# Performance work log

Measured on AMD Instinct MI355X. Metric: run time of the kernel, lower is better.

The kernel has to match this reference:

```python
import jax, jax.numpy as jnp
import numpy as np

N_NODES = 50000


def _sage_conv(x, src, dst, Wl, Wr, b):
    """SAGEConv with mean aggregation: lin_l(mean_j x_j) + lin_r(x_i) + b."""
    msgs = x[src]                                                # [E, Din] gather
    agg = jax.ops.segment_sum(msgs, dst, num_segments=N_NODES)  # [N, Din] scatter-add
    cnt = jax.ops.segment_sum(jnp.ones((src.shape[0], 1), x.dtype), dst,
                              num_segments=N_NODES)             # [N, 1]
    agg = agg / jnp.maximum(cnt, 1.0)                           # mean
    return agg @ Wl.T + x @ Wr.T + b                            # [N, Dout]


def setup_inputs() -> dict:
    key = jax.random.key(0)
    ks = jax.random.split(key, 8)
    d_in, d_h = 64, 128
    x = jax.random.normal(ks[0], (N_NODES, d_in), dtype=jnp.float32)
    edge_index = jax.random.randint(ks[1], (2, 800000), 0, N_NODES, dtype=jnp.int32)
    s1 = 1.0 / np.sqrt(d_in)
    s2 = 1.0 / np.sqrt(d_h)
    return {
        "x": x,
        "edge_index": edge_index,
        "Wl1": jax.random.normal(ks[2], (d_h, d_in), dtype=jnp.float32) * s1,
        "Wr1": jax.random.normal(ks[3], (d_h, d_in), dtype=jnp.float32) * s1,
        "b1": jnp.zeros((d_h,), dtype=jnp.float32),
        "Wl2": jax.random.normal(ks[4], (d_h, d_h), dtype=jnp.float32) * s2,
        "Wr2": jax.random.normal(ks[5], (d_h, d_h), dtype=jnp.float32) * s2,
        "b2": jnp.zeros((d_h,), dtype=jnp.float32),
    }


def reference(x, edge_index, Wl1, Wr1, b1, Wl2, Wr2, b2):
    src, dst = edge_index[0], edge_index[1]
    # layer 1: conv -> dropout(eval: identity) -> ReLU
    h = jax.nn.relu(_sage_conv(x, src, dst, Wl1, Wr1, b1))
    # layer 2
    h = jax.nn.relu(_sage_conv(h, src, dst, Wl2, Wr2, b2))
    return h
```

## Files before the change

### kernel.cpp

```cpp
#include <hip/hip_runtime.h>

#define N_NODES 50000
#define NBUCK 782
#define BCAP 2048
#define BSHIFT 11

typedef __attribute__((ext_vector_type(8))) short short8;
typedef __attribute__((ext_vector_type(4))) float floatx4;
typedef __attribute__((ext_vector_type(2))) float floatx2;
typedef __attribute__((ext_vector_type(2))) int intx2;

static __device__ __forceinline__ unsigned short f2bf(float f) {
  unsigned int u = __builtin_bit_cast(unsigned int, f);
  u += 0x7fff + ((u >> 16) & 1);
  return (unsigned short)(u >> 16);
}
static __device__ __forceinline__ void fp8x8_acc(intx2 v, floatx2* ac) {
  ac[0] += __builtin_amdgcn_cvt_pk_f32_fp8(v[0], false);
  ac[1] += __builtin_amdgcn_cvt_pk_f32_fp8(v[0], true);
  ac[2] += __builtin_amdgcn_cvt_pk_f32_fp8(v[1], false);
  ac[3] += __builtin_amdgcn_cvt_pk_f32_fp8(v[1], true);
}


__global__ void __launch_bounds__(512) prep_scatter(
    const float* __restrict__ x,
    const float* __restrict__ Wl1, const float* __restrict__ Wr1,
    const float* __restrict__ Wl2, const float* __restrict__ Wr2,
    unsigned short* __restrict__ xb, unsigned char* __restrict__ xq,
    unsigned short* __restrict__ W1, unsigned short* __restrict__ W2,
    const int* __restrict__ src, const int* __restrict__ dst,
    int* __restrict__ bucket_cur, int* __restrict__ buf, int E, int n) {
  const int t = threadIdx.x;
  const int gid = blockIdx.x * 512 + t;
  const int gsz = gridDim.x * 512;
  for (int i = gid; i < n * 16; i += gsz) {
    float4 v = ((const float4*)x)[i];
    unsigned int lo = (unsigned int)f2bf(v.x) | ((unsigned int)f2bf(v.y) << 16);
    unsigned int hi = (unsigned int)f2bf(v.z) | ((unsigned int)f2bf(v.w) << 16);
    ((uint2*)xb)[i] = make_uint2(lo, hi);
    int q = __builtin_amdgcn_cvt_pk_fp8_f32(v.x, v.y, 0, false);
    q = __builtin_amdgcn_cvt_pk_fp8_f32(v.z, v.w, q, true);
    ((int*)xq)[i] = q;
  }
  {
    unsigned char* h1q = xq + ((size_t)n + 1) * 64;
    if (gid < 16) ((int*)(xq + (size_t)n * 64))[gid] = 0;
    if (gid >= 16 && gid < 48) ((int*)(h1q + (size_t)n * 128))[gid - 16] = 0;
  }
  for (int i = gid; i < 128 * 128; i += gsz) {
    int c = i >> 7, k = i & 127;
    W1[i] = f2bf(k < 64 ? Wl1[c * 64 + k] : Wr1[c * 64 + k - 64]);
  }
  for (int i = gid; i < 128 * 256; i += gsz) {
    int c = i >> 8, k = i & 255;
    W2[i] = f2bf(k < 128 ? Wl2[c * 128 + k] : Wr2[c * 128 + k - 128]);
  }

  __shared__ int hist[NBUCK];
  __shared__ int base_s[NBUCK];
  for (int i = t; i < NBUCK; i += 512) hist[i] = 0;
  __syncthreads();
  int e0 = blockIdx.x * 4096;
  int sv[8], dv[8], bv[8];
#pragma unroll
  for (int p = 0; p < 8; ++p) {
    int e = e0 + p * 512 + t;
    if (e < E) {
      sv[p] = src[e];
      dv[p] = dst[e];
      bv[p] = dv[p] >> 6;
      atomicAdd(&hist[bv[p]], 1);
    } else bv[p] = -1;
  }
  __syncthreads();
  for (int i = t; i < NBUCK; i += 512) {
    int c = hist[i];
    base_s[i] = c > 0 ? atomicAdd(&bucket_cur[i], c) : 0;
  }
  __syncthreads();
  for (int i = t; i < NBUCK; i += 512) hist[i] = 0;
  __syncthreads();
#pragma unroll
  for (int p = 0; p < 8; ++p) {
    if (bv[p] >= 0) {
      int sub = base_s[bv[p]] + atomicAdd(&hist[bv[p]], 1);
      if (sub < BCAP) buf[(bv[p] << BSHIFT) + sub] = (sv[p] << 6) | (dv[p] & 63);
    }
  }
}


__global__ void __launch_bounds__(512, 6) csr_agg_gemm1(
    int* __restrict__ buf, const int* __restrict__ bucket_cur,
    int* __restrict__ row_start, int* __restrict__ row_cnt,
    const unsigned short* __restrict__ xb, const unsigned char* __restrict__ xq,
    const unsigned short* __restrict__ W1, const float* __restrict__ b1,
    unsigned short* __restrict__ h1, unsigned char* __restrict__ h1q, int n) {
  __shared__ int eb[BCAP];
  __shared__ int gsrc[BCAP];
  __shared__ __align__(16) unsigned short aggS[64 * 72];
  __shared__ int cnt[64];
  __shared__ int tmp[64];
  __shared__ int cur[64];
  const int t = threadIdx.x;
  const int b = blockIdx.x;
  const int node0 = b << 6;
  const int len = min(bucket_cur[b], BCAP);
  int* reg = buf + (b << BSHIFT);

  if (t < 64) cnt[t] = 0;
  __syncthreads();
  for (int i = t; i < len; i += 512) {
    int p = reg[i];
    eb[i] = p;
    atomicAdd(&cnt[p & 63], 1);
  }
  __syncthreads();
  if (t < 64) tmp[t] = (cnt[t] + 7) & ~7;
  __syncthreads();
#pragma unroll
  for (int off = 1; off < 64; off <<= 1) {
    int u = (t >= off && t < 64) ? tmp[t - off] : 0;
    __syncthreads();
    if (t < 64) tmp[t] += u;
    __syncthreads();
  }
  if (t < 64) {
    int c8 = (cnt[t] + 7) & ~7;
    int ex = tmp[t] - c8;
    cur[t] = ex;
    int nd = node0 + t;
    if (nd < n) {
      row_start[nd] = (b << BSHIFT) + ex;
      row_cnt[nd] = cnt[t];
    }
  }
  __syncthreads();
  for (int i = t; i < len; i += 512) {
    int p = eb[i];
    int sub = atomicAdd(&cur[p & 63], 1);
    int s = p >> 6;
    if (sub < BCAP) { gsrc[sub] = s; reg[sub] = s; }
  }
  __syncthreads();
  if (t < 64) {
    int c8 = (cnt[t] + 7) & ~7;
    int e1 = tmp[t];
    for (int j = e1 - c8 + cnt[t]; j < e1; ++j)
      if (j < BCAP) { gsrc[j] = n; reg[j] = n; }
  }
  __syncthreads();

  const int lane = t & 63;
  const int wv = t >> 6;
  const int eq = lane >> 3;
  const int cl = lane & 7;
#pragma unroll 1
  for (int p = 0; p < 4; ++p) {
    int locA = wv + p * 16;
    int locB = locA + 8;
    int cnA = cnt[locA], cnB = cnt[locB];
    int cpA = (cnA + 7) & ~7, cpB = (cnB + 7) & ~7;
    int baseA = tmp[locA] - cpA;
    int baseB = tmp[locB] - cpB;
    floatx2 aA[4], aB[4];
#pragma unroll
    for (int j = 0; j < 4; ++j) { aA[j] = (floatx2){0.f, 0.f}; aB[j] = (floatx2){0.f, 0.f}; }
    int mx = max(cpA, cpB);
    int sA = (0 < cpA) ? gsrc[baseA + eq] : n;
    int sB = (0 < cpB) ? gsrc[baseB + eq] : n;
    intx2 vA = *(const intx2*)(xq + (size_t)sA * 64 + cl * 8);
    intx2 vB = *(const intx2*)(xq + (size_t)sB * 64 + cl * 8);
    for (int e = 8; e < mx; e += 8) {
      int sA1 = (e < cpA) ? gsrc[baseA + e + eq] : n;
      int sB1 = (e < cpB) ? gsrc[baseB + e + eq] : n;
      intx2 vA1 = *(const intx2*)(xq + (size_t)sA1 * 64 + cl * 8);
      intx2 vB1 = *(const intx2*)(xq + (size_t)sB1 * 64 + cl * 8);
      fp8x8_acc(vA, aA);
      fp8x8_acc(vB, aB);
      vA = vA1; vB = vB1;
    }
    fp8x8_acc(vA, aA);
    fp8x8_acc(vB, aB);
    float rA[8], rB[8];
#pragma unroll
    for (int j = 0; j < 4; ++j) {
      rA[2 * j] = aA[j][0]; rA[2 * j + 1] = aA[j][1];
      rB[2 * j] = aB[j][0]; rB[2 * j + 1] = aB[j][1];
    }
#pragma unroll
    for (int j = 0; j < 8; ++j) {
      rA[j] += __shfl_xor(rA[j], 8, 64);
      rA[j] += __shfl_xor(rA[j], 16, 64);
      rA[j] += __shfl_xor(rA[j], 32, 64);
      rB[j] += __shfl_xor(rB[j], 8, 64);
      rB[j] += __shfl_xor(rB[j], 16, 64);
      rB[j] += __shfl_xor(rB[j], 32, 64);
    }
    if (eq == 0) {
      float invA = 1.0f / (float)max(cnA, 1);
      float invB = 1.0f / (float)max(cnB, 1);
      short8 oA, oB;
#pragma unroll
      for (int j = 0; j < 8; ++j) { oA[j] = (short)f2bf(rA[j] * invA); oB[j] = (short)f2bf(rB[j] * invB); }
      *(short8*)(aggS + locA * 72 + cl * 8) = oA;
      *(short8*)(aggS + locB * 72 + cl * 8) = oB;
    }
  }
  __syncthreads();

  const int m = lane & 15;
  const int q = lane >> 4;
  const int rw = (wv & 1) * 32;
  const int cw = (wv >> 1) * 32;
  floatx4 acc[2][2];
#pragma unroll
  for (int rt = 0; rt < 2; ++rt)
#pragma unroll
    for (int ct = 0; ct < 2; ++ct) acc[rt][ct] = (floatx4){0.f, 0.f, 0.f, 0.f};

  int ra = node0 + rw + m;      if (ra > n - 1) ra = n - 1;
  int rb = node0 + rw + 16 + m; if (rb > n - 1) rb = n - 1;
  const unsigned short* selfA0 = xb + (size_t)ra * 64 + q * 8;
  const unsigned short* selfA1 = xb + (size_t)rb * 64 + q * 8;
  const unsigned short* aggL0 = aggS + (rw + m) * 72 + q * 8;
  const unsigned short* aggL1 = aggS + (rw + 16 + m) * 72 + q * 8;
  const unsigned short* Wc0 = W1 + (size_t)(cw + m) * 128 + q * 8;
  const unsigned short* Wc1 = W1 + (size_t)(cw + 16 + m) * 128 + q * 8;

#pragma unroll
  for (int kc = 0; kc < 2; ++kc) {
    short8 a0 = *(const short8*)(aggL0 + kc * 32);
    short8 a1 = *(const short8*)(aggL1 + kc * 32);
    short8 w0 = *(const short8*)(Wc0 + kc * 32);
    short8 w1 = *(const short8*)(Wc1 + kc * 32);
    acc[0][0] = __builtin_amdgcn_mfma_f32_16x16x32_bf16(a0, w0, acc[0][0], 0, 0, 0);
    acc[0][1] = __builtin_amdgcn_mfma_f32_16x16x32_bf16(a0, w1, acc[0][1], 0, 0, 0);
    acc[1][0] = __builtin_amdgcn_mfma_f32_16x16x32_bf16(a1, w0, acc[1][0], 0, 0, 0);
    acc[1][1] = __builtin_amdgcn_mfma_f32_16x16x32_bf16(a1, w1, acc[1][1], 0, 0, 0);
  }
#pragma unroll
  for (int kc = 0; kc < 2; ++kc) {
    short8 a0 = *(const short8*)(selfA0 + kc * 32);
    short8 a1 = *(const short8*)(selfA1 + kc * 32);
    short8 w0 = *(const short8*)(Wc0 + 64 + kc * 32);
    short8 w1 = *(const short8*)(Wc1 + 64 + kc * 32);
    acc[0][0] = __builtin_amdgcn_mfma_f32_16x16x32_bf16(a0, w0, acc[0][0], 0, 0, 0);
    acc[0][1] = __builtin_amdgcn_mfma_f32_16x16x32_bf16(a0, w1, acc[0][1], 0, 0, 0);
    acc[1][0] = __builtin_amdgcn_mfma_f32_16x16x32_bf16(a1, w0, acc[1][0], 0, 0, 0);
    acc[1][1] = __builtin_amdgcn_mfma_f32_16x16x32_bf16(a1, w1, acc[1][1], 0, 0, 0);
  }

  float bv0 = b1[cw + m], bv1 = b1[cw + 16 + m];
#pragma unroll
  for (int rt = 0; rt < 2; ++rt) {
#pragma unroll
    for (int j = 0; j < 4; ++j) {
      int row = node0 + rw + rt * 16 + q * 4 + j;
      if (row < n) {
        float v0 = acc[rt][0][j] + bv0; v0 = v0 > 0.f ? v0 : 0.f;
        float v1 = acc[rt][1][j] + bv1; v1 = v1 > 0.f ? v1 : 0.f;
        h1[(size_t)row * 128 + cw + m] = f2bf(v0);
        h1[(size_t)row * 128 + cw + 16 + m] = f2bf(v1);
        h1q[(size_t)row * 128 + cw + m] =
            (unsigned char)__builtin_amdgcn_cvt_pk_fp8_f32(v0, v0, 0, false);
        h1q[(size_t)row * 128 + cw + 16 + m] =
            (unsigned char)__builtin_amdgcn_cvt_pk_fp8_f32(v1, v1, 0, false);
      }
    }
  }
}


__global__ void __launch_bounds__(512, 6) agg_gemm2(
    const unsigned short* __restrict__ h1, const unsigned char* __restrict__ h1q,
    const int* __restrict__ row_start, const int* __restrict__ row_cnt,
    const int* __restrict__ buf, const unsigned short* __restrict__ W2,
    const float* __restrict__ b2, float* __restrict__ out, int n) {
  __shared__ int gsrcS[BCAP];
  __shared__ __align__(16) unsigned short aggS[64 * 136];
  const int t = threadIdx.x;
  const int lane = t & 63;
  const int wv = t >> 6;
  const int node0 = blockIdx.x << 6;

  {
    const int4* b4 = (const int4*)(buf + ((size_t)blockIdx.x << BSHIFT));
    ((int4*)gsrcS)[t] = b4[t];
  }
  __syncthreads();

  const int eq = lane >> 4;
  const int cl = lane & 15;
#pragma unroll 1
  for (int lp = 0; lp < 4; ++lp) {
    int locA = wv + lp * 16;
    int locB = locA + 8;
    int ndA = node0 + locA, ndB = node0 + locB;
    int cnA = 0, stA = 0, cnB = 0, stB = 0;
    if (ndA < n) { cnA = row_cnt[ndA]; stA = row_start[ndA] - (blockIdx.x << BSHIFT); }
    if (ndB < n) { cnB = row_cnt[ndB]; stB = row_start[ndB] - (blockIdx.x << BSHIFT); }
    int cpA = (cnA + 7) & ~7, cpB = (cnB + 7) & ~7;
    int mx = max(cpA, cpB);
    floatx2 aA[4], aB[4];
#pragma unroll
    for (int j = 0; j < 4; ++j) { aA[j] = (floatx2){0.f, 0.f}; aB[j] = (floatx2){0.f, 0.f}; }
    int sA0 = (0 < cpA) ? gsrcS[stA + eq] : n;
    int sA1 = (0 < cpA) ? gsrcS[stA + 4 + eq] : n;
    int sB0 = (0 < cpB) ? gsrcS[stB + eq] : n;
    int sB1 = (0 < cpB) ? gsrcS[stB + 4 + eq] : n;
    intx2 vA0 = *(const intx2*)(h1q + (size_t)sA0 * 128 + cl * 8);
    intx2 vA1 = *(const intx2*)(h1q + (size_t)sA1 * 128 + cl * 8);
    intx2 vB0 = *(const intx2*)(h1q + (size_t)sB0 * 128 + cl * 8);
    intx2 vB1 = *(const intx2*)(h1q + (size_t)sB1 * 128 + cl * 8);
    for (int e = 8; e < mx; e += 8) {
      int tA0 = (e < cpA) ? gsrcS[stA + e + eq] : n;
      int tA1 = (e < cpA) ? gsrcS[stA + e + 4 + eq] : n;
      int tB0 = (e < cpB) ? gsrcS[stB + e + eq] : n;
      int tB1 = (e < cpB) ? gsrcS[stB + e + 4 + eq] : n;
      intx2 wA0 = *(const intx2*)(h1q + (size_t)tA0 * 128 + cl * 8);
      intx2 wA1 = *(const intx2*)(h1q + (size_t)tA1 * 128 + cl * 8);
      intx2 wB0 = *(const intx2*)(h1q + (size_t)tB0 * 128 + cl * 8);
      intx2 wB1 = *(const intx2*)(h1q + (size_t)tB1 * 128 + cl * 8);
      fp8x8_acc(vA0, aA); fp8x8_acc(vA1, aA);
      fp8x8_acc(vB0, aB); fp8x8_acc(vB1, aB);
      vA0 = wA0; vA1 = wA1; vB0 = wB0; vB1 = wB1;
    }
    fp8x8_acc(vA0, aA); fp8x8_acc(vA1, aA);
    fp8x8_acc(vB0, aB); fp8x8_acc(vB1, aB);

    float rA[8], rB[8];
#pragma unroll
    for (int j = 0; j < 4; ++j) {
      rA[2 * j] = aA[j][0]; rA[2 * j + 1] = aA[j][1];
      rB[2 * j] = aB[j][0]; rB[2 * j + 1] = aB[j][1];
    }
#pragma unroll
    for (int j = 0; j < 8; ++j) {
      rA[j] += __shfl_xor(rA[j], 16, 64);
      rA[j] += __shfl_xor(rA[j], 32, 64);
      rB[j] += __shfl_xor(rB[j], 16, 64);
      rB[j] += __shfl_xor(rB[j], 32, 64);
    }
    if (eq == 0) {
      float invA = 1.0f / (float)max(cnA, 1);
      float invB = 1.0f / (float)max(cnB, 1);
      short8 oA, oB;
#pragma unroll
      for (int j = 0; j < 8; ++j) { oA[j] = (short)f2bf(rA[j] * invA); oB[j] = (short)f2bf(rB[j] * invB); }
      *(short8*)(aggS + locA * 136 + cl * 8) = oA;
      *(short8*)(aggS + locB * 136 + cl * 8) = oB;
    }
  }
  __syncthreads();

  const int m = lane & 15;
  const int q = lane >> 4;
  const int rw = (wv & 1) * 32;
  const int cw = (wv >> 1) * 32;
  floatx4 acc[2][2];
#pragma unroll
  for (int rt = 0; rt < 2; ++rt)
#pragma unroll
    for (int ct = 0; ct < 2; ++ct) acc[rt][ct] = (floatx4){0.f, 0.f, 0.f, 0.f};

  int ra = node0 + rw + m;      if (ra > n - 1) ra = n - 1;
  int rb = node0 + rw + 16 + m; if (rb > n - 1) rb = n - 1;
  const unsigned short* selfA0 = h1 + (size_t)ra * 128 + q * 8;
  const unsigned short* selfA1 = h1 + (size_t)rb * 128 + q * 8;
  const unsigned short* aggL0 = aggS + (rw + m) * 136 + q * 8;
  const unsigned short* aggL1 = aggS + (rw + 16 + m) * 136 + q * 8;
  const unsigned short* Wc0 = W2 + (size_t)(cw + m) * 256 + q * 8;
  const unsigned short* Wc1 = W2 + (size_t)(cw + 16 + m) * 256 + q * 8;

#pragma unroll
  for (int kc = 0; kc < 4; ++kc) {
    short8 a0 = *(const short8*)(aggL0 + kc * 32);
    short8 a1 = *(const short8*)(aggL1 + kc * 32);
    short8 w0 = *(const short8*)(Wc0 + kc * 32);
    short8 w1 = *(const short8*)(Wc1 + kc * 32);
    acc[0][0] = __builtin_amdgcn_mfma_f32_16x16x32_bf16(a0, w0, acc[0][0], 0, 0, 0);
    acc[0][1] = __builtin_amdgcn_mfma_f32_16x16x32_bf16(a0, w1, acc[0][1], 0, 0, 0);
    acc[1][0] = __builtin_amdgcn_mfma_f32_16x16x32_bf16(a1, w0, acc[1][0], 0, 0, 0);
    acc[1][1] = __builtin_amdgcn_mfma_f32_16x16x32_bf16(a1, w1, acc[1][1], 0, 0, 0);
  }
#pragma unroll
  for (int kc = 0; kc < 4; ++kc) {
    short8 a0 = *(const short8*)(selfA0 + kc * 32);
    short8 a1 = *(const short8*)(selfA1 + kc * 32);
    short8 w0 = *(const short8*)(Wc0 + 128 + kc * 32);
    short8 w1 = *(const short8*)(Wc1 + 128 + kc * 32);
    acc[0][0] = __builtin_amdgcn_mfma_f32_16x16x32_bf16(a0, w0, acc[0][0], 0, 0, 0);
    acc[0][1] = __builtin_amdgcn_mfma_f32_16x16x32_bf16(a0, w1, acc[0][1], 0, 0, 0);
    acc[1][0] = __builtin_amdgcn_mfma_f32_16x16x32_bf16(a1, w0, acc[1][0], 0, 0, 0);
    acc[1][1] = __builtin_amdgcn_mfma_f32_16x16x32_bf16(a1, w1, acc[1][1], 0, 0, 0);
  }

  float bv0 = b2[cw + m], bv1 = b2[cw + 16 + m];
#pragma unroll
  for (int rt = 0; rt < 2; ++rt) {
#pragma unroll
    for (int j = 0; j < 4; ++j) {
      int row = node0 + rw + rt * 16 + q * 4 + j;
      if (row < n) {
        float v0 = acc[rt][0][j] + bv0; v0 = v0 > 0.f ? v0 : 0.f;
        float v1 = acc[rt][1][j] + bv1; v1 = v1 > 0.f ? v1 : 0.f;
        out[(size_t)row * 128 + cw + m] = v0;
        out[(size_t)row * 128 + cw + 16 + m] = v1;
      }
    }
  }
}


extern "C" void kernel_launch(void* const* d_in, const int* in_sizes, int n_in,
                              void* d_out, int out_size, void* d_ws, size_t ws_size,
                              hipStream_t stream) {
  const int N = N_NODES;
  const int E = in_sizes[1] / 2;
  const float* x   = (const float*)d_in[0];
  const int*   src = (const int*)d_in[1];
  const int*   dst = src + E;
  const float* Wl1 = (const float*)d_in[2];
  const float* Wr1 = (const float*)d_in[3];
  const float* b1  = (const float*)d_in[4];
  const float* Wl2 = (const float*)d_in[5];
  const float* Wr2 = (const float*)d_in[6];
  const float* b2  = (const float*)d_in[7];
  float* out = (float*)d_out;

  unsigned short* xb = (unsigned short*)d_ws;
  unsigned short* h1 = xb + (size_t)N * 64;
  unsigned short* W1 = h1 + (size_t)N * 128;
  unsigned short* W2 = W1 + 128 * 128;
  int* row_start  = (int*)(W2 + 128 * 256);
  int* row_cnt    = row_start + N;
  int* bucket_cur = row_cnt + N;
  int* buf        = bucket_cur + 784;
  unsigned char* xq  = (unsigned char*)(buf + (size_t)NBUCK * BCAP);
  unsigned char* h1q = xq + ((size_t)N + 1) * 64;

  (void)hipMemsetAsync(bucket_cur, 0, NBUCK * sizeof(int), stream);
  int sb = (E + 4095) / 4096;
  prep_scatter<<<sb, 512, 0, stream>>>(x, Wl1, Wr1, Wl2, Wr2, xb, xq, W1, W2,
                                       src, dst, bucket_cur, buf, E, N);
  csr_agg_gemm1<<<NBUCK, 512, 0, stream>>>(buf, bucket_cur, row_start, row_cnt,
                                           xb, xq, W1, b1, h1, h1q, N);
  agg_gemm2<<<NBUCK, 512, 0, stream>>>(h1, h1q, row_start, row_cnt, buf, W2, b2, out, N);
}
```

Baseline: 185.1 us.

## Halve node buckets to 32 nodes with 256-thread blocks and 4-way gather ILP

Buckets now cover 32 destination nodes instead of 64, which doubles the block count to 1563 and halves the threads per block to 256 for both aggregation+GEMM kernels. Each wave now aggregates four nodes at once instead of two, giving more independent gather loads in flight. The GEMM tiling is remapped so each wave covers all 32 rows for a 32-column slice. Bucket capacity drops to 1024 edges, which leaves less headroom before edges overflow and get dropped for heavily connected buckets.

```diff
diff --git a/kernel.cpp b/kernel.cpp
--- a/kernel.cpp
+++ b/kernel.cpp
@@ -1,9 +1,9 @@
 #include <hip/hip_runtime.h>
 
 #define N_NODES 50000
-#define NBUCK 782
-#define BCAP 2048
-#define BSHIFT 11
+#define NBUCK 1563
+#define BCAP 1024
+#define BSHIFT 10
 
 typedef __attribute__((ext_vector_type(8))) short short8;
 typedef __attribute__((ext_vector_type(4))) float floatx4;
@@ -69,7 +69,7 @@
     if (e < E) {
       sv[p] = src[e];
       dv[p] = dst[e];
-      bv[p] = dv[p] >> 6;
+      bv[p] = dv[p] >> 5;
       atomicAdd(&hist[bv[p]], 1);
     } else bv[p] = -1;
   }
@@ -85,13 +85,13 @@
   for (int p = 0; p < 8; ++p) {
     if (bv[p] >= 0) {
       int sub = base_s[bv[p]] + atomicAdd(&hist[bv[p]], 1);
-      if (sub < BCAP) buf[(bv[p] << BSHIFT) + sub] = (sv[p] << 6) | (dv[p] & 63);
-    }
-  }
-}
-
-
-__global__ void __launch_bounds__(512, 6) csr_agg_gemm1(
+      if (sub < BCAP) buf[(bv[p] << BSHIFT) + sub] = (sv[p] << 5) | (dv[p] & 31);
+    }
+  }
+}
+
+
+__global__ void __launch_bounds__(256) csr_agg_gemm1(
     int* __restrict__ buf, const int* __restrict__ bucket_cur,
     int* __restrict__ row_start, int* __restrict__ row_cnt,
     const unsigned short* __restrict__ xb, const unsigned char* __restrict__ xq,
@@ -99,34 +99,34 @@
     unsigned short* __restrict__ h1, unsigned char* __restrict__ h1q, int n) {
   __shared__ int eb[BCAP];
   __shared__ int gsrc[BCAP];
-  __shared__ __align__(16) unsigned short aggS[64 * 72];
-  __shared__ int cnt[64];
-  __shared__ int tmp[64];
-  __shared__ int cur[64];
+  __shared__ __align__(16) unsigned short aggS[32 * 72];
+  __shared__ int cnt[32];
+  __shared__ int tmp[32];
+  __shared__ int cur[32];
   const int t = threadIdx.x;
   const int b = blockIdx.x;
-  const int node0 = b << 6;
+  const int node0 = b << 5;
   const int len = min(bucket_cur[b], BCAP);
   int* reg = buf + (b << BSHIFT);
 
-  if (t < 64) cnt[t] = 0;
-  __syncthreads();
-  for (int i = t; i < len; i += 512) {
+  if (t < 32) cnt[t] = 0;
+  __syncthreads();
+  for (int i = t; i < len; i += 256) {
     int p = reg[i];
     eb[i] = p;
-    atomicAdd(&cnt[p & 63], 1);
-  }
-  __syncthreads();
-  if (t < 64) tmp[t] = (cnt[t] + 7) & ~7;
-  __syncthreads();
-#pragma unroll
-  for (int off = 1; off < 64; off <<= 1) {
-    int u = (t >= off && t < 64) ? tmp[t - off] : 0;
+    atomicAdd(&cnt[p & 31], 1);
+  }
+  __syncthreads();
+  if (t < 32) tmp[t] = (cnt[t] + 7) & ~7;
+  __syncthreads();
+#pragma unroll
+  for (int off = 1; off < 32; off <<= 1) {
+    int u = (t >= off && t < 32) ? tmp[t - off] : 0;
     __syncthreads();
-    if (t < 64) tmp[t] += u;
+    if (t < 32) tmp[t] += u;
     __syncthreads();
   }
-  if (t < 64) {
+  if (t < 32) {
     int c8 = (cnt[t] + 7) & ~7;
     int ex = tmp[t] - c8;
     cur[t] = ex;
@@ -137,14 +137,14 @@
     }
   }
   __syncthreads();
-  for (int i = t; i < len; i += 512) {
+  for (int i = t; i < len; i += 256) {
     int p = eb[i];
-    int sub = atomicAdd(&cur[p & 63], 1);
-    int s = p >> 6;
+    int sub = atomicAdd(&cur[p & 31], 1);
+    int s = p >> 5;
     if (sub < BCAP) { gsrc[sub] = s; reg[sub] = s; }
   }
   __syncthreads();
-  if (t < 64) {
+  if (t < 32) {
     int c8 = (cnt[t] + 7) & ~7;
     int e1 = tmp[t];
     for (int j = e1 - c8 + cnt[t]; j < e1; ++j)
@@ -157,75 +157,79 @@
   const int eq = lane >> 3;
   const int cl = lane & 7;
 #pragma unroll 1
-  for (int p = 0; p < 4; ++p) {
-    int locA = wv + p * 16;
-    int locB = locA + 8;
-    int cnA = cnt[locA], cnB = cnt[locB];
-    int cpA = (cnA + 7) & ~7, cpB = (cnB + 7) & ~7;
-    int baseA = tmp[locA] - cpA;
-    int baseB = tmp[locB] - cpB;
-    floatx2 aA[4], aB[4];
-#pragma unroll
-    for (int j = 0; j < 4; ++j) { aA[j] = (floatx2){0.f, 0.f}; aB[j] = (floatx2){0.f, 0.f}; }
-    int mx = max(cpA, cpB);
-    int sA = (0 < cpA) ? gsrc[baseA + eq] : n;
-    int sB = (0 < cpB) ? gsrc[baseB + eq] : n;
-    intx2 vA = *(const intx2*)(xq + (size_t)sA * 64 + cl * 8);
-    intx2 vB = *(const intx2*)(xq + (size_t)sB * 64 + cl * 8);
+  for (int g = 0; g < 2; ++g) {
+    int loc0 = wv * 8 + g * 4;
+    int cn0 = cnt[loc0], cn1 = cnt[loc0 + 1], cn2 = cnt[loc0 + 2], cn3 = cnt[loc0 + 3];
+    int cp0 = (cn0 + 7) & ~7, cp1 = (cn1 + 7) & ~7, cp2 = (cn2 + 7) & ~7, cp3 = (cn3 + 7) & ~7;
+    int ba0 = tmp[loc0] - cp0, ba1 = tmp[loc0 + 1] - cp1,
+        ba2 = tmp[loc0 + 2] - cp2, ba3 = tmp[loc0 + 3] - cp3;
+    floatx2 a0[4], a1[4], a2[4], a3[4];
+#pragma unroll
+    for (int j = 0; j < 4; ++j) {
+      a0[j] = (floatx2){0.f, 0.f}; a1[j] = (floatx2){0.f, 0.f};
+      a2[j] = (floatx2){0.f, 0.f}; a3[j] = (floatx2){0.f, 0.f};
+    }
+    int mx = max(max(cp0, cp1), max(cp2, cp3));
+    int s0 = (0 < cp0) ? gsrc[ba0 + eq] : n;
+    int s1 = (0 < cp1) ? gsrc[ba1 + eq] : n;
+    int s2 = (0 < cp2) ? gsrc[ba2 + eq] : n;
+    int s3 = (0 < cp3) ? gsrc[ba3 + eq] : n;
+    intx2 v0 = *(const intx2*)(xq + (size_t)s0 * 64 + cl * 8);
+    intx2 v1 = *(const intx2*)(xq + (size_t)s1 * 64 + cl * 8);
+    intx2 v2 = *(const intx2*)(xq + (size_t)s2 * 64 + cl * 8);
+    intx2 v3 = *(const intx2*)(xq + (size_t)s3 * 64 + cl * 8);
     for (int e = 8; e < mx; e += 8) {
-      int sA1 = (e < cpA) ? gsrc[baseA + e + eq] : n;
-      int sB1 = (e < cpB) ? gsrc[baseB + e + eq] : n;
-      intx2 vA1 = *(const intx2*)(xq + (size_t)sA1 * 64 + cl * 8);
-      intx2 vB1 = *(const intx2*)(xq + (size_t)sB1 * 64 + cl * 8);
-      fp8x8_acc(vA, aA);
-      fp8x8_acc(vB, aB);
-      vA = vA1; vB = vB1;
-    }
-    fp8x8_acc(vA, aA);
-    fp8x8_acc(vB, aB);
-    float rA[8], rB[8];
-#pragma unroll
-    for (int j = 0; j < 4; ++j) {
-      rA[2 * j] = aA[j][0]; rA[2 * j + 1] = aA[j][1];
-      rB[2 * j] = aB[j][0]; rB[2 * j + 1] = aB[j][1];
-    }
-#pragma unroll
-    for (int j = 0; j < 8; ++j) {
-      rA[j] += __shfl_xor(rA[j], 8, 64);
-      rA[j] += __shfl_xor(rA[j], 16, 64);
-      rA[j] += __shfl_xor(rA[j], 32, 64);
-      rB[j] += __shfl_xor(rB[j], 8, 64);
-      rB[j] += __shfl_xor(rB[j], 16, 64);
-      rB[j] += __shfl_xor(rB[j], 32, 64);
-    }
-    if (eq == 0) {
-      float invA = 1.0f / (float)max(cnA, 1);
-      float invB = 1.0f / (float)max(cnB, 1);
-      short8 oA, oB;
-#pragma unroll
-      for (int j = 0; j < 8; ++j) { oA[j] = (short)f2bf(rA[j] * invA); oB[j] = (short)f2bf(rB[j] * invB); }
-      *(short8*)(aggS + locA * 72 + cl * 8) = oA;
-      *(short8*)(aggS + locB * 72 + cl * 8) = oB;
+      int u0 = (e < cp0) ? gsrc[ba0 + e + eq] : n;
+      int u1 = (e < cp1) ? gsrc[ba1 + e + eq] : n;
+      int u2 = (e < cp2) ? gsrc[ba2 + e + eq] : n;
+      int u3 = (e < cp3) ? gsrc[ba3 + e + eq] : n;
+      intx2 w0 = *(const intx2*)(xq + (size_t)u0 * 64 + cl * 8);
+      intx2 w1 = *(const intx2*)(xq + (size_t)u1 * 64 + cl * 8);
+      intx2 w2 = *(const intx2*)(xq + (size_t)u2 * 64 + cl * 8);
+      intx2 w3 = *(const intx2*)(xq + (size_t)u3 * 64 + cl * 8);
+      fp8x8_acc(v0, a0); fp8x8_acc(v1, a1); fp8x8_acc(v2, a2); fp8x8_acc(v3, a3);
+      v0 = w0; v1 = w1; v2 = w2; v3 = w3;
+    }
+    fp8x8_acc(v0, a0); fp8x8_acc(v1, a1); fp8x8_acc(v2, a2); fp8x8_acc(v3, a3);
+#pragma unroll
+    for (int i = 0; i < 4; ++i) {
+      floatx2* ai = (i == 0) ? a0 : (i == 1) ? a1 : (i == 2) ? a2 : a3;
+      int cni = (i == 0) ? cn0 : (i == 1) ? cn1 : (i == 2) ? cn2 : cn3;
+      float r[8];
+#pragma unroll
+      for (int j = 0; j < 4; ++j) { r[2 * j] = ai[j][0]; r[2 * j + 1] = ai[j][1]; }
+#pragma unroll
+      for (int j = 0; j < 8; ++j) {
+        r[j] += __shfl_xor(r[j], 8, 64);
+        r[j] += __shfl_xor(r[j], 16, 64);
+        r[j] += __shfl_xor(r[j], 32, 64);
+      }
+      if (eq == 0) {
+        float inv = 1.0f / (float)max(cni, 1);
+        short8 o;
+#pragma unroll
+        for (int j = 0; j < 8; ++j) o[j] = (short)f2bf(r[j] * inv);
+        *(short8*)(aggS + (loc0 + i) * 72 + cl * 8) = o;
+      }
     }
   }
   __syncthreads();
 
   const int m = lane & 15;
   const int q = lane >> 4;
-  const int rw = (wv & 1) * 32;
-  const int cw = (wv >> 1) * 32;
+  const int cw = wv * 32;
   floatx4 acc[2][2];
 #pragma unroll
   for (int rt = 0; rt < 2; ++rt)
 #pragma unroll
     for (int ct = 0; ct < 2; ++ct) acc[rt][ct] = (floatx4){0.f, 0.f, 0.f, 0.f};
 
-  int ra = node0 + rw + m;      if (ra > n - 1) ra = n - 1;
-  int rb = node0 + rw + 16 + m; if (rb > n - 1) rb = n - 1;
+  int ra = node0 + m;      if (ra > n - 1) ra = n - 1;
+  int rb = node0 + 16 + m; if (rb > n - 1) rb = n - 1;
   const unsigned short* selfA0 = xb + (size_t)ra * 64 + q * 8;
   const unsigned short* selfA1 = xb + (size_t)rb * 64 + q * 8;
-  const unsigned short* aggL0 = aggS + (rw + m) * 72 + q * 8;
-  const unsigned short* aggL1 = aggS + (rw + 16 + m) * 72 + q * 8;
+  const unsigned short* aggL0 = aggS + m * 72 + q * 8;
+  const unsigned short* aggL1 = aggS + (16 + m) * 72 + q * 8;
   const unsigned short* Wc0 = W1 + (size_t)(cw + m) * 128 + q * 8;
   const unsigned short* Wc1 = W1 + (size_t)(cw + 16 + m) * 128 + q * 8;
 
@@ -257,7 +261,7 @@
   for (int rt = 0; rt < 2; ++rt) {
 #pragma unroll
     for (int j = 0; j < 4; ++j) {
-      int row = node0 + rw + rt * 16 + q * 4 + j;
+      int row = node0 + rt * 16 + q * 4 + j;
       if (row < n) {
         float v0 = acc[rt][0][j] + bv0; v0 = v0 > 0.f ? v0 : 0.f;
         float v1 = acc[rt][1][j] + bv1; v1 = v1 > 0.f ? v1 : 0.f;
@@ -273,17 +277,17 @@
 }
 
 
-__global__ void __launch_bounds__(512, 6) agg_gemm2(
+__global__ void __launch_bounds__(256) agg_gemm2(
     const unsigned short* __restrict__ h1, const unsigned char* __restrict__ h1q,
     const int* __restrict__ row_start, const int* __restrict__ row_cnt,
     const int* __restrict__ buf, const unsigned short* __restrict__ W2,
     const float* __restrict__ b2, float* __restrict__ out, int n) {
   __shared__ int gsrcS[BCAP];
-  __shared__ __align__(16) unsigned short aggS[64 * 136];
+  __shared__ __align__(16) unsigned short aggS[32 * 136];
   const int t = threadIdx.x;
   const int lane = t & 63;
   const int wv = t >> 6;
-  const int node0 = blockIdx.x << 6;
+  const int node0 = blockIdx.x << 5;
 
   {
     const int4* b4 = (const int4*)(buf + ((size_t)blockIdx.x << BSHIFT));
@@ -294,83 +298,84 @@
   const int eq = lane >> 4;
   const int cl = lane & 15;
 #pragma unroll 1
-  for (int lp = 0; lp < 4; ++lp) {
-    int locA = wv + lp * 16;
-    int locB = locA + 8;
-    int ndA = node0 + locA, ndB = node0 + locB;
-    int cnA = 0, stA = 0, cnB = 0, stB = 0;
-    if (ndA < n) { cnA = row_cnt[ndA]; stA = row_start[ndA] - (blockIdx.x << BSHIFT); }
-    if (ndB < n) { cnB = row_cnt[ndB]; stB = row_start[ndB] - (blockIdx.x << BSHIFT); }
-    int cpA = (cnA + 7) & ~7, cpB = (cnB + 7) & ~7;
-    int mx = max(cpA, cpB);
-    floatx2 aA[4], aB[4];
-#pragma unroll
-    for (int j = 0; j < 4; ++j) { aA[j] = (floatx2){0.f, 0.f}; aB[j] = (floatx2){0.f, 0.f}; }
-    int sA0 = (0 < cpA) ? gsrcS[stA + eq] : n;
-    int sA1 = (0 < cpA) ? gsrcS[stA + 4 + eq] : n;
-    int sB0 = (0 < cpB) ? gsrcS[stB + eq] : n;
-    int sB1 = (0 < cpB) ? gsrcS[stB + 4 + eq] : n;
-    intx2 vA0 = *(const intx2*)(h1q + (size_t)sA0 * 128 + cl * 8);
-    intx2 vA1 = *(const intx2*)(h1q + (size_t)sA1 * 128 + cl * 8);
-    intx2 vB0 = *(const intx2*)(h1q + (size_t)sB0 * 128 + cl * 8);
-    intx2 vB1 = *(const intx2*)(h1q + (size_t)sB1 * 128 + cl * 8);
-    for (int e = 8; e < mx; e += 8) {
-      int tA0 = (e < cpA) ? gsrcS[stA + e + eq] : n;
-      int tA1 = (e < cpA) ? gsrcS[stA + e + 4 + eq] : n;
-      int tB0 = (e < cpB) ? gsrcS[stB + e + eq] : n;
-      int tB1 = (e < cpB) ? gsrcS[stB + e + 4 + eq] : n;
-      intx2 wA0 = *(const intx2*)(h1q + (size_t)tA0 * 128 + cl * 8);
-      intx2 wA1 = *(const intx2*)(h1q + (size_t)tA1 * 128 + cl * 8);
-      intx2 wB0 = *(const intx2*)(h1q + (size_t)tB0 * 128 + cl * 8);
-      intx2 wB1 = *(const intx2*)(h1q + (size_t)tB1 * 128 + cl * 8);
-      fp8x8_acc(vA0, aA); fp8x8_acc(vA1, aA);
-      fp8x8_acc(vB0, aB); fp8x8_acc(vB1, aB);
-      vA0 = wA0; vA1 = wA1; vB0 = wB0; vB1 = wB1;
-    }
-    fp8x8_acc(vA0, aA); fp8x8_acc(vA1, aA);
-    fp8x8_acc(vB0, aB); fp8x8_acc(vB1, aB);
-
-    float rA[8], rB[8];
+  for (int g = 0; g < 2; ++g) {
+    int loc0 = wv * 8 + g * 4;
+    int cn0 = 0, st0 = 0, cn1 = 0, st1 = 0, cn2 = 0, st2 = 0, cn3 = 0, st3 = 0;
+    {
+      int nd = node0 + loc0;
+      int boff = blockIdx.x << BSHIFT;
+      if (nd < n)     { cn0 = row_cnt[nd];     st0 = row_start[nd] - boff; }
+      if (nd + 1 < n) { cn1 = row_cnt[nd + 1]; st1 = row_start[nd + 1] - boff; }
+      if (nd + 2 < n) { cn2 = row_cnt[nd + 2]; st2 = row_start[nd + 2] - boff; }
+      if (nd + 3 < n) { cn3 = row_cnt[nd + 3]; st3 = row_start[nd + 3] - boff; }
+    }
+    int cp0 = (cn0 + 7) & ~7, cp1 = (cn1 + 7) & ~7, cp2 = (cn2 + 7) & ~7, cp3 = (cn3 + 7) & ~7;
+    int mx = max(max(cp0, cp1), max(cp2, cp3));
+    floatx2 a0[4], a1[4], a2[4], a3[4];
 #pragma unroll
     for (int j = 0; j < 4; ++j) {
-      rA[2 * j] = aA[j][0]; rA[2 * j + 1] = aA[j][1];
-      rB[2 * j] = aB[j][0]; rB[2 * j + 1] = aB[j][1];
-    }
-#pragma unroll
-    for (int j = 0; j < 8; ++j) {
-      rA[j] += __shfl_xor(rA[j], 16, 64);
-      rA[j] += __shfl_xor(rA[j], 32, 64);
-      rB[j] += __shfl_xor(rB[j], 16, 64);
-      rB[j] += __shfl_xor(rB[j], 32, 64);
-    }
-    if (eq == 0) {
-      float invA = 1.0f / (float)max(cnA, 1);
-      float invB = 1.0f / (float)max(cnB, 1);
-      short8 oA, oB;
-#pragma unroll
-      for (int j = 0; j < 8; ++j) { oA[j] = (short)f2bf(rA[j] * invA); oB[j] = (short)f2bf(rB[j] * invB); }
-      *(short8*)(aggS + locA * 136 + cl * 8) = oA;
-      *(short8*)(aggS + locB * 136 + cl * 8) = oB;
+      a0[j] = (floatx2){0.f, 0.f}; a1[j] = (floatx2){0.f, 0.f};
+      a2[j] = (floatx2){0.f, 0.f}; a3[j] = (floatx2){0.f, 0.f};
+    }
+    int s0 = (0 < cp0) ? gsrcS[st0 + eq] : n;
+    int s1 = (0 < cp1) ? gsrcS[st1 + eq] : n;
+    int s2 = (0 < cp2) ? gsrcS[st2 + eq] : n;
+    int s3 = (0 < cp3) ? gsrcS[st3 + eq] : n;
+    intx2 v0 = *(const intx2*)(h1q + (size_t)s0 * 128 + cl * 8);
+    intx2 v1 = *(const intx2*)(h1q + (size_t)s1 * 128 + cl * 8);
+    intx2 v2 = *(const intx2*)(h1q + (size_t)s2 * 128 + cl * 8);
+    intx2 v3 = *(const intx2*)(h1q + (size_t)s3 * 128 + cl * 8);
+    for (int e = 4; e < mx; e += 4) {
+      int u0 = (e < cp0) ? gsrcS[st0 + e + eq] : n;
+      int u1 = (e < cp1) ? gsrcS[st1 + e + eq] : n;
+      int u2 = (e < cp2) ? gsrcS[st2 + e + eq] : n;
+      int u3 = (e < cp3) ? gsrcS[st3 + e + eq] : n;
+      intx2 w0 = *(const intx2*)(h1q + (size_t)u0 * 128 + cl * 8);
+      intx2 w1 = *(const intx2*)(h1q + (size_t)u1 * 128 + cl * 8);
+      intx2 w2 = *(const intx2*)(h1q + (size_t)u2 * 128 + cl * 8);
+      intx2 w3 = *(const intx2*)(h1q + (size_t)u3 * 128 + cl * 8);
+      fp8x8_acc(v0, a0); fp8x8_acc(v1, a1); fp8x8_acc(v2, a2); fp8x8_acc(v3, a3);
+      v0 = w0; v1 = w1; v2 = w2; v3 = w3;
+    }
+    fp8x8_acc(v0, a0); fp8x8_acc(v1, a1); fp8x8_acc(v2, a2); fp8x8_acc(v3, a3);
+#pragma unroll
+    for (int i = 0; i < 4; ++i) {
+      floatx2* ai = (i == 0) ? a0 : (i == 1) ? a1 : (i == 2) ? a2 : a3;
+      int cni = (i == 0) ? cn0 : (i == 1) ? cn1 : (i == 2) ? cn2 : cn3;
+      float r[8];
+#pragma unroll
+      for (int j = 0; j < 4; ++j) { r[2 * j] = ai[j][0]; r[2 * j + 1] = ai[j][1]; }
+#pragma unroll
+      for (int j = 0; j < 8; ++j) {
+        r[j] += __shfl_xor(r[j], 16, 64);
+        r[j] += __shfl_xor(r[j], 32, 64);
+      }
+      if (eq == 0) {
+        float inv = 1.0f / (float)max(cni, 1);
+        short8 o;
+#pragma unroll
+        for (int j = 0; j < 8; ++j) o[j] = (short)f2bf(r[j] * inv);
+        *(short8*)(aggS + (loc0 + i) * 136 + cl * 8) = o;
+      }
     }
   }
   __syncthreads();
 
   const int m = lane & 15;
   const int q = lane >> 4;
-  const int rw = (wv & 1) * 32;
-  const int cw = (wv >> 1) * 32;
+  const int cw = wv * 32;
   floatx4 acc[2][2];
 #pragma unroll
   for (int rt = 0; rt < 2; ++rt)
 #pragma unroll
     for (int ct = 0; ct < 2; ++ct) acc[rt][ct] = (floatx4){0.f, 0.f, 0.f, 0.f};
 
-  int ra = node0 + rw + m;      if (ra > n - 1) ra = n - 1;
-  int rb = node0 + rw + 16 + m; if (rb > n - 1) rb = n - 1;
+  int ra = node0 + m;      if (ra > n - 1) ra = n - 1;
+  int rb = node0 + 16 + m; if (rb > n - 1) rb = n - 1;
   const unsigned short* selfA0 = h1 + (size_t)ra * 128 + q * 8;
   const unsigned short* selfA1 = h1 + (size_t)rb * 128 + q * 8;
-  const unsigned short* aggL0 = aggS + (rw + m) * 136 + q * 8;
-  const unsigned short* aggL1 = aggS + (rw + 16 + m) * 136 + q * 8;
+  const unsigned short* aggL0 = aggS + m * 136 + q * 8;
+  const unsigned short* aggL1 = aggS + (16 + m) * 136 + q * 8;
   const unsigned short* Wc0 = W2 + (size_t)(cw + m) * 256 + q * 8;
   const unsigned short* Wc1 = W2 + (size_t)(cw + 16 + m) * 256 + q * 8;
 
@@ -402,7 +407,7 @@
   for (int rt = 0; rt < 2; ++rt) {
 #pragma unroll
     for (int j = 0; j < 4; ++j) {
-      int row = node0 + rw + rt * 16 + q * 4 + j;
+      int row = node0 + rt * 16 + q * 4 + j;
       if (row < n) {
         float v0 = acc[rt][0][j] + bv0; v0 = v0 > 0.f ? v0 : 0.f;
         float v1 = acc[rt][1][j] + bv1; v1 = v1 > 0.f ? v1 : 0.f;
@@ -437,7 +442,7 @@
   int* row_start  = (int*)(W2 + 128 * 256);
   int* row_cnt    = row_start + N;
   int* bucket_cur = row_cnt + N;
-  int* buf        = bucket_cur + 784;
+  int* buf        = bucket_cur + 1564;
   unsigned char* xq  = (unsigned char*)(buf + (size_t)NBUCK * BCAP);
   unsigned char* h1q = xq + ((size_t)N + 1) * 64;
 
@@ -445,7 +450,7 @@
   int sb = (E + 4095) / 4096;
   prep_scatter<<<sb, 512, 0, stream>>>(x, Wl1, Wr1, Wl2, Wr2, xb, xq, W1, W2,
                                        src, dst, bucket_cur, buf, E, N);
-  csr_agg_gemm1<<<NBUCK, 512, 0, stream>>>(buf, bucket_cur, row_start, row_cnt,
+  csr_agg_gemm1<<<NBUCK, 256, 0, stream>>>(buf, bucket_cur, row_start, row_cnt,
                                            xb, xq, W1, b1, h1, h1q, N);
-  agg_gemm2<<<NBUCK, 512, 0, stream>>>(h1, h1q, row_start, row_cnt, buf, W2, b2, out, N);
-}
+  agg_gemm2<<<NBUCK, 256, 0, stream>>>(h1, h1q, row_start, row_cnt, buf, W2, b2, out, N);
+}
```

New measurement: 184.1 us. About the same (-0.6%).

## Split fused prep/scatter and CSR/agg kernels into separate launches

Applied to the files above, without the earlier changes.

Splits the fused preprocessing and scatter kernel into a cast kernel and a scatter kernel, and splits the CSR-build plus layer-1 aggregation/GEMM kernel into a CSR build kernel and a separate aggregation GEMM kernel. The new aggregation kernel reloads the bucket's source list from global memory into LDS and reads per-row start and count from global arrays. The goal is to shrink LDS and register pressure in the heavy aggregation kernel so more blocks fit per CU, at the cost of two extra launches and extra global traffic for the CSR data.

```diff
diff --git a/kernel.cpp b/kernel.cpp
--- a/kernel.cpp
+++ b/kernel.cpp
@@ -23,16 +23,14 @@
 }
 
 
-__global__ void __launch_bounds__(512) prep_scatter(
+__global__ void __launch_bounds__(512) prep_cast(
     const float* __restrict__ x,
     const float* __restrict__ Wl1, const float* __restrict__ Wr1,
     const float* __restrict__ Wl2, const float* __restrict__ Wr2,
     unsigned short* __restrict__ xb, unsigned char* __restrict__ xq,
     unsigned short* __restrict__ W1, unsigned short* __restrict__ W2,
-    const int* __restrict__ src, const int* __restrict__ dst,
-    int* __restrict__ bucket_cur, int* __restrict__ buf, int E, int n) {
-  const int t = threadIdx.x;
-  const int gid = blockIdx.x * 512 + t;
+    unsigned char* __restrict__ h1q, int n) {
+  const int gid = blockIdx.x * 512 + threadIdx.x;
   const int gsz = gridDim.x * 512;
   for (int i = gid; i < n * 16; i += gsz) {
     float4 v = ((const float4*)x)[i];
@@ -43,11 +41,8 @@
     q = __builtin_amdgcn_cvt_pk_fp8_f32(v.z, v.w, q, true);
     ((int*)xq)[i] = q;
   }
-  {
-    unsigned char* h1q = xq + ((size_t)n + 1) * 64;
-    if (gid < 16) ((int*)(xq + (size_t)n * 64))[gid] = 0;
-    if (gid >= 16 && gid < 48) ((int*)(h1q + (size_t)n * 128))[gid - 16] = 0;
-  }
+  if (gid < 16) ((int*)(xq + (size_t)n * 64))[gid] = 0;
+  if (gid >= 16 && gid < 48) ((int*)(h1q + (size_t)n * 128))[gid - 16] = 0;
   for (int i = gid; i < 128 * 128; i += gsz) {
     int c = i >> 7, k = i & 127;
     W1[i] = f2bf(k < 64 ? Wl1[c * 64 + k] : Wr1[c * 64 + k - 64]);
@@ -56,9 +51,15 @@
     int c = i >> 8, k = i & 255;
     W2[i] = f2bf(k < 128 ? Wl2[c * 128 + k] : Wr2[c * 128 + k - 128]);
   }
-
+}
+
+
+__global__ void __launch_bounds__(512) scatter(
+    const int* __restrict__ src, const int* __restrict__ dst,
+    int* __restrict__ bucket_cur, int* __restrict__ buf, int E) {
   __shared__ int hist[NBUCK];
   __shared__ int base_s[NBUCK];
+  const int t = threadIdx.x;
   for (int i = t; i < NBUCK; i += 512) hist[i] = 0;
   __syncthreads();
   int e0 = blockIdx.x * 4096;
@@ -91,15 +92,10 @@
 }
 
 
-__global__ void __launch_bounds__(512, 6) csr_agg_gemm1(
+__global__ void __launch_bounds__(512) csr_build(
     int* __restrict__ buf, const int* __restrict__ bucket_cur,
-    int* __restrict__ row_start, int* __restrict__ row_cnt,
-    const unsigned short* __restrict__ xb, const unsigned char* __restrict__ xq,
-    const unsigned short* __restrict__ W1, const float* __restrict__ b1,
-    unsigned short* __restrict__ h1, unsigned char* __restrict__ h1q, int n) {
+    int* __restrict__ row_start, int* __restrict__ row_cnt, int n) {
   __shared__ int eb[BCAP];
-  __shared__ int gsrc[BCAP];
-  __shared__ __align__(16) unsigned short aggS[64 * 72];
   __shared__ int cnt[64];
   __shared__ int tmp[64];
   __shared__ int cur[64];
@@ -107,7 +103,7 @@
   const int b = blockIdx.x;
   const int node0 = b << 6;
   const int len = min(bucket_cur[b], BCAP);
-  int* reg = buf + (b << BSHIFT);
+  int* reg = buf + ((size_t)b << BSHIFT);
 
   if (t < 64) cnt[t] = 0;
   __syncthreads();
@@ -140,41 +136,60 @@
   for (int i = t; i < len; i += 512) {
     int p = eb[i];
     int sub = atomicAdd(&cur[p & 63], 1);
-    int s = p >> 6;
-    if (sub < BCAP) { gsrc[sub] = s; reg[sub] = s; }
+    if (sub < BCAP) reg[sub] = p >> 6;
   }
   __syncthreads();
   if (t < 64) {
     int c8 = (cnt[t] + 7) & ~7;
     int e1 = tmp[t];
     for (int j = e1 - c8 + cnt[t]; j < e1; ++j)
-      if (j < BCAP) { gsrc[j] = n; reg[j] = n; }
-  }
-  __syncthreads();
-
+      if (j < BCAP) reg[j] = n;
+  }
+}
+
+
+__global__ void __launch_bounds__(512, 6) agg_gemm1(
+    const unsigned short* __restrict__ xb, const unsigned char* __restrict__ xq,
+    const int* __restrict__ row_start, const int* __restrict__ row_cnt,
+    const int* __restrict__ buf, const unsigned short* __restrict__ W1,
+    const float* __restrict__ b1,
+    unsigned short* __restrict__ h1, unsigned char* __restrict__ h1q, int n) {
+  __shared__ int gsrcS[BCAP];
+  __shared__ __align__(16) unsigned short aggS[64 * 72];
+  const int t = threadIdx.x;
   const int lane = t & 63;
   const int wv = t >> 6;
+  const int node0 = blockIdx.x << 6;
+  const int boff = blockIdx.x << BSHIFT;
+
+  {
+    const int4* b4 = (const int4*)(buf + ((size_t)blockIdx.x << BSHIFT));
+    ((int4*)gsrcS)[t] = b4[t];
+  }
+  __syncthreads();
+
   const int eq = lane >> 3;
   const int cl = lane & 7;
 #pragma unroll 1
   for (int p = 0; p < 4; ++p) {
     int locA = wv + p * 16;
     int locB = locA + 8;
-    int cnA = cnt[locA], cnB = cnt[locB];
+    int ndA = node0 + locA, ndB = node0 + locB;
+    int cnA = 0, stA = 0, cnB = 0, stB = 0;
+    if (ndA < n) { cnA = row_cnt[ndA]; stA = row_start[ndA] - boff; }
+    if (ndB < n) { cnB = row_cnt[ndB]; stB = row_start[ndB] - boff; }
     int cpA = (cnA + 7) & ~7, cpB = (cnB + 7) & ~7;
-    int baseA = tmp[locA] - cpA;
-    int baseB = tmp[locB] - cpB;
     floatx2 aA[4], aB[4];
 #pragma unroll
     for (int j = 0; j < 4; ++j) { aA[j] = (floatx2){0.f, 0.f}; aB[j] = (floatx2){0.f, 0.f}; }
     int mx = max(cpA, cpB);
-    int sA = (0 < cpA) ? gsrc[baseA + eq] : n;
-    int sB = (0 < cpB) ? gsrc[baseB + eq] : n;
+    int sA = (0 < cpA) ? gsrcS[stA + eq] : n;
+    int sB = (0 < cpB) ? gsrcS[stB + eq] : n;
     intx2 vA = *(const intx2*)(xq + (size_t)sA * 64 + cl * 8);
     intx2 vB = *(const intx2*)(xq + (size_t)sB * 64 + cl * 8);
     for (int e = 8; e < mx; e += 8) {
-      int sA1 = (e < cpA) ? gsrc[baseA + e + eq] : n;
-      int sB1 = (e < cpB) ? gsrc[baseB + e + eq] : n;
+      int sA1 = (e < cpA) ? gsrcS[stA + e + eq] : n;
+      int sB1 = (e < cpB) ? gsrcS[stB + e + eq] : n;
       intx2 vA1 = *(const intx2*)(xq + (size_t)sA1 * 64 + cl * 8);
       intx2 vB1 = *(const intx2*)(xq + (size_t)sB1 * 64 + cl * 8);
       fp8x8_acc(vA, aA);
@@ -442,10 +457,11 @@
   unsigned char* h1q = xq + ((size_t)N + 1) * 64;
 
   (void)hipMemsetAsync(bucket_cur, 0, NBUCK * sizeof(int), stream);
+  prep_cast<<<391, 512, 0, stream>>>(x, Wl1, Wr1, Wl2, Wr2, xb, xq, W1, W2, h1q, N);
   int sb = (E + 4095) / 4096;
-  prep_scatter<<<sb, 512, 0, stream>>>(x, Wl1, Wr1, Wl2, Wr2, xb, xq, W1, W2,
-                                       src, dst, bucket_cur, buf, E, N);
-  csr_agg_gemm1<<<NBUCK, 512, 0, stream>>>(buf, bucket_cur, row_start, row_cnt,
-                                           xb, xq, W1, b1, h1, h1q, N);
+  scatter<<<sb, 512, 0, stream>>>(src, dst, bucket_cur, buf, E);
+  csr_build<<<NBUCK, 512, 0, stream>>>(buf, bucket_cur, row_start, row_cnt, N);
+  agg_gemm1<<<NBUCK, 512, 0, stream>>>(xb, xq, row_start, row_cnt, buf, W1, b1,
+                                       h1, h1q, N);
   agg_gemm2<<<NBUCK, 512, 0, stream>>>(h1, h1q, row_start, row_cnt, buf, W2, b2, out, N);
 }
```

After: 193.4 us. 4.5% more time.
